# Performance work log

Measured on AMD Instinct MI355X. Metric: run time of the kernel, lower is better.

Reference implementation:

```python
import jax, jax.numpy as jnp
import numpy as np
import math

D_PAIR = 64
N_HEADS = 4
D_HEAD = D_PAIR // N_HEADS


def setup_inputs() -> dict:
    key = jax.random.key(0)
    ks = jax.random.split(key, 9)
    B, L, D = 2, 256, D_PAIR
    s = 1.0 / math.sqrt(D)
    return {
        "z": jax.random.normal(ks[0], (B, L, L, D), dtype=jnp.float32),
        "ln_scale": jnp.ones((D,), jnp.float32),
        "ln_bias": jnp.zeros((D,), jnp.float32),
        "Wq": jax.random.normal(ks[1], (D, D), jnp.float32) * s,
        "Wk": jax.random.normal(ks[2], (D, D), jnp.float32) * s,
        "Wv": jax.random.normal(ks[3], (D, D), jnp.float32) * s,
        "Wg": jax.random.normal(ks[4], (D, D), jnp.float32) * s,
        "bg": jax.random.normal(ks[5], (D,), jnp.float32) * 0.02,
        "Wo": jax.random.normal(ks[6], (D, D), jnp.float32) * s,
        "bo": jax.random.normal(ks[7], (D,), jnp.float32) * 0.02,
    }


def _layernorm(x, scale, bias, eps=1e-5):
    mu = jnp.mean(x, axis=-1, keepdims=True)
    var = jnp.var(x, axis=-1, keepdims=True)
    return (x - mu) * jax.lax.rsqrt(var + eps) * scale + bias


def reference(z, ln_scale, ln_bias, Wq, Wk, Wv, Wg, bg, Wo, bo):
    B, L, _, D = z.shape
    H, Dh = N_HEADS, D_HEAD
    zn = _layernorm(z, ln_scale, ln_bias)
    # torch Linear(no bias): x @ W.T
    Q = (zn @ Wq.T).reshape(B, L, L, H, Dh)
    K = (zn @ Wk.T).reshape(B, L, L, H, Dh)
    V = (zn @ Wv.T).reshape(B, L, L, H, Dh)
    scale = 1.0 / math.sqrt(Dh)
    # row-wise attention: for each row l, attend over column index j
    attn = jnp.einsum("blihd,bljhd->blhij", Q, K) * scale  # [B,L,H,L,L]
    attn = jax.nn.softmax(attn, axis=-1)
    out = jnp.einsum("blhij,bljhd->blihd", attn, V).reshape(B, L, L, D)
    gate = jax.nn.sigmoid(zn @ Wg.T + bg)
    out = gate * out
    return out @ Wo.T + bo
```

## Files before the change

kernel.cpp:

```cpp
#include <hip/hip_runtime.h>
#include <hip/hip_bf16.h>
#include <math.h>


typedef __attribute__((ext_vector_type(4))) float f32x4;
typedef __attribute__((ext_vector_type(8))) short s16x8;
typedef __attribute__((ext_vector_type(4))) short s16x4;

#define MFMA16(a, b, c) __builtin_amdgcn_mfma_f32_16x16x32_bf16((a), (b), (c), 0, 0, 0)

__device__ __forceinline__ f32x4 mfma16b(s16x4 a, s16x4 b, f32x4 c) {
#if __has_builtin(__builtin_amdgcn_mfma_f32_16x16x16bf16_1k)
    return __builtin_amdgcn_mfma_f32_16x16x16bf16_1k(a, b, c, 0, 0, 0);
#elif __has_builtin(__builtin_amdgcn_mfma_f32_16x16x16_bf16)
    return __builtin_amdgcn_mfma_f32_16x16x16_bf16(a, b, c, 0, 0, 0);
#else
    f32x4 d;
    asm volatile("s_nop 1\n\t"
                 "v_mfma_f32_16x16x16_bf16 %0, %1, %2, %3\n\t"
                 "s_nop 7\n\t"
                 "s_nop 7"
                 : "=v"(d) : "v"(a), "v"(b), "v"(c));
    return d;
#endif
}

__device__ __forceinline__ float exp2a(float x) {
    float r;
    asm("v_exp_f32 %0, %1" : "=v"(r) : "v"(x));
    return r;
}
__device__ __forceinline__ float rcpa(float x) {
    float r;
    asm("v_rcp_f32 %0, %1" : "=v"(r) : "v"(x));
    return r;
}

__device__ __forceinline__ unsigned pk2(float a, float b) {
    union { __hip_bfloat162 h; unsigned u; } c;
    float2 t; t.x = a; t.y = b;
    c.h = __float22bfloat162_rn(t);
    return c.u;
}
__device__ __forceinline__ s16x8 cvt8(const float* p) {
    union { unsigned u[4]; s16x8 v; } r;
    r.u[0] = pk2(p[0], p[1]); r.u[1] = pk2(p[2], p[3]);
    r.u[2] = pk2(p[4], p[5]); r.u[3] = pk2(p[6], p[7]);
    return r.v;
}
__device__ __forceinline__ s16x4 cvt4(const float* p) {
    union { unsigned u[2]; s16x4 v; } r;
    r.u[0] = pk2(p[0], p[1]); r.u[1] = pk2(p[2], p[3]);
    return r.v;
}

static constexpr int ZNL = 0;
static constexpr int KSH = 16384;
static constexpr int VT  = 21504;
static constexpr int LDS_EL = 25728;

__global__ __launch_bounds__(256, 2)
void ka_all(const float* __restrict__ z, const float* __restrict__ ln_s,
            const float* __restrict__ ln_b, const float* __restrict__ Wq,
            const float* __restrict__ Wk, const float* __restrict__ Wv,
            const float* __restrict__ Wg, const float* __restrict__ bg,
            const float* __restrict__ Wo, const float* __restrict__ bo,
            float* __restrict__ out)
{
    __shared__ __align__(16) short lds[LDS_EL];
    const int tid = threadIdx.x, lane = tid & 63, w = tid >> 6;
    const int n16 = lane & 15, quad = lane >> 4;
    const int bl = blockIdx.x;
    const int wsl = w * 4096;
    const int wrows = w * 64;

    {
        float zn[64];
        const float4* zp4 = (const float4*)(z + ((size_t)bl * 256 + tid) * 64);
        #pragma unroll
        for (int gq = 0; gq < 16; ++gq) {
            float4 v4 = zp4[gq];
            zn[gq * 4 + 0] = v4.x; zn[gq * 4 + 1] = v4.y;
            zn[gq * 4 + 2] = v4.z; zn[gq * 4 + 3] = v4.w;
        }
        float mu = 0.f;
        #pragma unroll
        for (int k = 0; k < 64; ++k) mu += zn[k];
        mu *= (1.f / 64.f);
        float va = 0.f;
        #pragma unroll
        for (int k = 0; k < 64; ++k) { float d = zn[k] - mu; va += d * d; }
        const float rs = rsqrtf(va * (1.f / 64.f) + 1e-5f);
        #pragma unroll
        for (int k = 0; k < 64; ++k) zn[k] = (zn[k] - mu) * rs * ln_s[k] + ln_b[k];
        const int lr = lane;
        #pragma unroll
        for (int gq = 0; gq < 8; ++gq) {
            union { unsigned u[4]; s16x8 v; } pkv;
            pkv.u[0] = pk2(zn[gq * 8 + 0], zn[gq * 8 + 1]);
            pkv.u[1] = pk2(zn[gq * 8 + 2], zn[gq * 8 + 3]);
            pkv.u[2] = pk2(zn[gq * 8 + 4], zn[gq * 8 + 5]);
            pkv.u[3] = pk2(zn[gq * 8 + 6], zn[gq * 8 + 7]);
            *(s16x8*)&lds[ZNL + wsl + (lr >> 4) * 1024 + (lr & 15) * 64
                          + ((gq ^ (lr & 7)) * 8)] = pkv.v;
        }
    }

    constexpr float QS  = 0.25f;
    constexpr float L2E = 1.44269504088896340736f;
    s16x4 ones4;
    {
        union { unsigned u[2]; s16x4 v; } c;
        c.u[0] = 0x3F803F80u; c.u[1] = 0x3F803F80u;
        ones4 = c.v;
    }

    f32x4 acc_out[4][4];
    #pragma unroll
    for (int qt = 0; qt < 4; ++qt)
        #pragma unroll
        for (int nt = 0; nt < 4; ++nt) acc_out[qt][nt] = {};

    for (int h = 0; h < 4; ++h) {
        s16x8 bq[2], bk[2], bv[2], bgf[2];
        #pragma unroll
        for (int ks = 0; ks < 2; ++ks) {
            size_t off = (size_t)(h * 16 + n16) * 64 + ks * 32 + quad * 8;
            bq[ks] = cvt8(Wq + off);  bk[ks] = cvt8(Wk + off);
            bv[ks] = cvt8(Wv + off);  bgf[ks] = cvt8(Wg + off);
        }
        const float4 bg4 = *(const float4*)(bg + h * 16 + quad * 4);

        float g4t[4][4];
        s16x4 qa4[4];
        #pragma unroll
        for (int t = 0; t < 4; ++t) {
            s16x8 zn0 = *(const s16x8*)&lds[ZNL + wsl + t * 1024 + n16 * 64
                                            + ((quad ^ (n16 & 7)) * 8)];
            s16x8 zn1 = *(const s16x8*)&lds[ZNL + wsl + t * 1024 + n16 * 64
                                            + (((4 + quad) ^ (n16 & 7)) * 8)];
            f32x4 aq = {}, ak = {}, av = {}, ag = {};
            aq = MFMA16(bq[0], zn0, aq);  aq = MFMA16(bq[1], zn1, aq);
            ak = MFMA16(bk[0], zn0, ak);  ak = MFMA16(bk[1], zn1, ak);
            ag = MFMA16(bgf[0], zn0, ag); ag = MFMA16(bgf[1], zn1, ag);
            av = MFMA16(zn0, bv[0], av);  av = MFMA16(zn1, bv[1], av);
            {
                union { unsigned u[2]; s16x4 v; } q;
                q.u[0] = pk2(aq[0] * QS, aq[1] * QS);
                q.u[1] = pk2(aq[2] * QS, aq[3] * QS);
                qa4[t] = q.v;
            }
            {
                uint2 p = {pk2(ak[0], ak[1]), pk2(ak[2], ak[3])};
                *(uint2*)&lds[KSH + (wrows + t * 16 + n16) * 20 + quad * 4] = p;
            }
            {
                uint2 p = {pk2(av[0], av[1]), pk2(av[2], av[3])};
                *(uint2*)&lds[VT + n16 * 264 + (wrows + t * 16 + quad * 4)] = p;
            }
            #pragma unroll
            for (int r = 0; r < 4; ++r) {
                float x = ag[r] + bg4[r];
                g4t[t][r] = rcpa(1.f + exp2a(x * -L2E));
            }
        }
        __syncthreads();

        f32x4 o4[4], lacc[4];
        #pragma unroll
        for (int qt = 0; qt < 4; ++qt) { o4[qt] = {}; lacc[qt] = {}; }
        const int kbase = KSH + n16 * 20 + quad * 4;
        const int vbase = VT + n16 * 264 + quad * 4;
        for (int ch = 0; ch < 8; ++ch) {
            #pragma unroll
            for (int jtl = 0; jtl < 2; ++jtl) {
                const int jt = ch * 2 + jtl;
                s16x4 kf = *(const s16x4*)&lds[kbase + jt * 320];
                s16x4 vf = *(const s16x4*)&lds[vbase + jt * 16];
                #pragma unroll
                for (int qt = 0; qt < 4; ++qt) {
                    f32x4 zc = {};
                    f32x4 s = mfma16b(kf, qa4[qt], zc);
                    float e0 = exp2a(s[0] * L2E), e1 = exp2a(s[1] * L2E);
                    float e2 = exp2a(s[2] * L2E), e3 = exp2a(s[3] * L2E);
                    union { unsigned u[2]; s16x4 v; } pb;
                    pb.u[0] = pk2(e0, e1); pb.u[1] = pk2(e2, e3);
                    o4[qt]   = mfma16b(vf, pb.v, o4[qt]);
                    lacc[qt] = mfma16b(ones4, pb.v, lacc[qt]);
                }
            }
        }

        s16x4 goB[4];
        #pragma unroll
        for (int qt = 0; qt < 4; ++qt) {
            const float l = (lacc[qt][0] + lacc[qt][1]) * 0.5f;
            const float inv = rcpa(l);
            float g0 = g4t[qt][0] * o4[qt][0] * inv;
            float g1 = g4t[qt][1] * o4[qt][1] * inv;
            float g2 = g4t[qt][2] * o4[qt][2] * inv;
            float g3 = g4t[qt][3] * o4[qt][3] * inv;
            union { unsigned u[2]; s16x4 v; } pb;
            pb.u[0] = pk2(g0, g1); pb.u[1] = pk2(g2, g3);
            goB[qt] = pb.v;
        }
        #pragma unroll
        for (int nt = 0; nt < 4; ++nt) {
            s16x4 wof = cvt4(Wo + (size_t)(nt * 16 + n16) * 64 + h * 16 + quad * 4);
            #pragma unroll
            for (int qt = 0; qt < 4; ++qt)
                acc_out[qt][nt] = mfma16b(wof, goB[qt], acc_out[qt][nt]);
        }
        __syncthreads();
    }

    #pragma unroll
    for (int nt = 0; nt < 4; ++nt) {
        const float4 b4 = *(const float4*)(bo + nt * 16 + quad * 4);
        f32x4 b4v; b4v[0] = b4.x; b4v[1] = b4.y; b4v[2] = b4.z; b4v[3] = b4.w;
        #pragma unroll
        for (int qt = 0; qt < 4; ++qt) {
            f32x4 v = acc_out[qt][nt] + b4v;
            *(f32x4*)&out[((size_t)bl * 256 + wrows + qt * 16 + n16) * 64
                          + nt * 16 + quad * 4] = v;
        }
    }
}

extern "C" void kernel_launch(void* const* d_in, const int* in_sizes, int n_in,
                              void* d_out, int out_size, void* d_ws, size_t ws_size,
                              hipStream_t stream) {
    const float* z  = (const float*)d_in[0];
    const float* ls = (const float*)d_in[1];
    const float* lb = (const float*)d_in[2];
    const float* Wq = (const float*)d_in[3];
    const float* Wk = (const float*)d_in[4];
    const float* Wv = (const float*)d_in[5];
    const float* Wg = (const float*)d_in[6];
    const float* bg = (const float*)d_in[7];
    const float* Wo = (const float*)d_in[8];
    const float* bo = (const float*)d_in[9];
    float* out = (float*)d_out;

    hipLaunchKernelGGL(ka_all, dim3(512), dim3(256), 0, stream,
                       z, ls, lb, Wq, Wk, Wv, Wg, bg, Wo, bo, out);
}
```

Baseline: 143.8 us.

## Split heads across two wave groups per block and reduce outputs via LDS

Doubles the block to 512 threads so two groups of four waves each process two of the four heads in parallel over the same row, each with its own K/V LDS region. Only the first group computes LayerNorm into shared memory. Each group accumulates a partial output projection, and the two partials are summed through LDS before the bias is added and the result stored. This adds parallelism per row and halves the serial head loop, at the cost of more LDS per block, an extra reduction pass, and tighter register limits under launch_bounds(512,4).

```diff
diff --git a/kernel.cpp b/kernel.cpp
--- a/kernel.cpp
+++ b/kernel.cpp
@@ -55,11 +55,10 @@
 }
 
 static constexpr int ZNL = 0;
-static constexpr int KSH = 16384;
-static constexpr int VT  = 21504;
-static constexpr int LDS_EL = 25728;
-
-__global__ __launch_bounds__(256, 2)
+static constexpr int KSHB = 16384;
+static constexpr int LDS_EL = 35072;
+
+__global__ __launch_bounds__(512, 4)
 void ka_all(const float* __restrict__ z, const float* __restrict__ ln_s,
             const float* __restrict__ ln_b, const float* __restrict__ Wq,
             const float* __restrict__ Wk, const float* __restrict__ Wv,
@@ -69,12 +68,15 @@
 {
     __shared__ __align__(16) short lds[LDS_EL];
     const int tid = threadIdx.x, lane = tid & 63, w = tid >> 6;
+    const int wg = w >> 2, wl = w & 3;
     const int n16 = lane & 15, quad = lane >> 4;
     const int bl = blockIdx.x;
-    const int wsl = w * 4096;
-    const int wrows = w * 64;
-
-    {
+    const int wsl = wl * 4096;
+    const int wrows = wl * 64;
+    const int KSHg = KSHB + wg * 9344;
+    const int VTg  = KSHg + 5120;
+
+    if (w < 4) {
         float zn[64];
         const float4* zp4 = (const float4*)(z + ((size_t)bl * 256 + tid) * 64);
         #pragma unroll
@@ -105,6 +107,7 @@
                           + ((gq ^ (lr & 7)) * 8)] = pkv.v;
         }
     }
+    __syncthreads();
 
     constexpr float QS  = 0.25f;
     constexpr float L2E = 1.44269504088896340736f;
@@ -121,7 +124,8 @@
         #pragma unroll
         for (int nt = 0; nt < 4; ++nt) acc_out[qt][nt] = {};
 
-    for (int h = 0; h < 4; ++h) {
+    for (int hh = 0; hh < 2; ++hh) {
+        const int h = wg * 2 + hh;
         s16x8 bq[2], bk[2], bv[2], bgf[2];
         #pragma unroll
         for (int ks = 0; ks < 2; ++ks) {
@@ -152,11 +156,11 @@
             }
             {
                 uint2 p = {pk2(ak[0], ak[1]), pk2(ak[2], ak[3])};
-                *(uint2*)&lds[KSH + (wrows + t * 16 + n16) * 20 + quad * 4] = p;
+                *(uint2*)&lds[KSHg + (wrows + t * 16 + n16) * 20 + quad * 4] = p;
             }
             {
                 uint2 p = {pk2(av[0], av[1]), pk2(av[2], av[3])};
-                *(uint2*)&lds[VT + n16 * 264 + (wrows + t * 16 + quad * 4)] = p;
+                *(uint2*)&lds[VTg + n16 * 264 + (wrows + t * 16 + quad * 4)] = p;
             }
             #pragma unroll
             for (int r = 0; r < 4; ++r) {
@@ -169,8 +173,8 @@
         f32x4 o4[4], lacc[4];
         #pragma unroll
         for (int qt = 0; qt < 4; ++qt) { o4[qt] = {}; lacc[qt] = {}; }
-        const int kbase = KSH + n16 * 20 + quad * 4;
-        const int vbase = VT + n16 * 264 + quad * 4;
+        const int kbase = KSHg + n16 * 20 + quad * 4;
+        const int vbase = VTg + n16 * 264 + quad * 4;
         for (int ch = 0; ch < 8; ++ch) {
             #pragma unroll
             for (int jtl = 0; jtl < 2; ++jtl) {
@@ -214,15 +218,28 @@
         __syncthreads();
     }
 
-    #pragma unroll
-    for (int nt = 0; nt < 4; ++nt) {
-        const float4 b4 = *(const float4*)(bo + nt * 16 + quad * 4);
-        f32x4 b4v; b4v[0] = b4.x; b4v[1] = b4.y; b4v[2] = b4.z; b4v[3] = b4.w;
-        #pragma unroll
-        for (int qt = 0; qt < 4; ++qt) {
-            f32x4 v = acc_out[qt][nt] + b4v;
-            *(f32x4*)&out[((size_t)bl * 256 + wrows + qt * 16 + n16) * 64
-                          + nt * 16 + quad * 4] = v;
+    float* red = (float*)lds;
+    if (wg == 1) {
+        #pragma unroll
+        for (int qt = 0; qt < 4; ++qt)
+            #pragma unroll
+            for (int nt = 0; nt < 4; ++nt)
+                *(f32x4*)&red[(wrows + qt * 16 + n16) * 68 + nt * 16 + quad * 4] =
+                    acc_out[qt][nt];
+    }
+    __syncthreads();
+    if (wg == 0) {
+        #pragma unroll
+        for (int nt = 0; nt < 4; ++nt) {
+            const float4 b4 = *(const float4*)(bo + nt * 16 + quad * 4);
+            f32x4 b4v; b4v[0] = b4.x; b4v[1] = b4.y; b4v[2] = b4.z; b4v[3] = b4.w;
+            #pragma unroll
+            for (int qt = 0; qt < 4; ++qt) {
+                f32x4 o = *(f32x4*)&red[(wrows + qt * 16 + n16) * 68 + nt * 16 + quad * 4];
+                f32x4 v = acc_out[qt][nt] + o + b4v;
+                *(f32x4*)&out[((size_t)bl * 256 + wrows + qt * 16 + n16) * 64
+                              + nt * 16 + quad * 4] = v;
+            }
         }
     }
 }
@@ -242,6 +259,6 @@
     const float* bo = (const float*)d_in[9];
     float* out = (float*)d_out;
 
-    hipLaunchKernelGGL(ka_all, dim3(512), dim3(256), 0, stream,
+    hipLaunchKernelGGL(ka_all, dim3(512), dim3(512), 0, stream,
                        z, ls, lb, Wq, Wk, Wv, Wg, bg, Wo, bo, out);
 }
```

Measured after the change: 155.0 us. 1.08x slower.
